# Optimization experiments

Measured on AMD Instinct MI355X. Metric: run time of the kernel, lower is better.

The kernel has to match this reference:

```python
import jax, jax.numpy as jnp
import numpy as np

B, L, D = 128, 196, 1024  # batch, att_size, rnn_size


def setup_inputs() -> dict:
    key = jax.random.key(0)
    ks = jax.random.split(key, 11)
    s = 1.0 / np.sqrt(D)
    return {
        "x": jax.random.normal(ks[0], (B, D), jnp.float32),
        "att": jax.random.normal(ks[1], (B, L, D), jnp.float32),
        "h": jax.random.normal(ks[2], (B, D), jnp.float32),
        "W_a2a": jax.random.uniform(ks[3], (D, D), jnp.float32, -s, s),
        "b_a2a": jax.random.uniform(ks[4], (D,), jnp.float32, -s, s),
        "W_h2a": jax.random.uniform(ks[5], (D, D), jnp.float32, -s, s),
        "b_h2a": jax.random.uniform(ks[6], (D,), jnp.float32, -s, s),
        "W_i2a": jax.random.uniform(ks[7], (D, D), jnp.float32, -s, s),
        "b_i2a": jax.random.uniform(ks[8], (D,), jnp.float32, -s, s),
        "W_d2d": jax.random.uniform(ks[9], (D,), jnp.float32, -s, s),
        "b_d2d": jax.random.uniform(ks[10], (), jnp.float32, -s, s),
    }


def reference(x, att, h, W_a2a, b_a2a, W_h2a, b_h2a, W_i2a, b_i2a, W_d2d, b_d2d):
    # att_v_1: [B, L, D]
    att_v = jnp.einsum('bld,ed->ble', att, W_a2a) + b_a2a
    att_h = (h @ W_h2a.T + b_h2a)[:, None, :]   # [B, 1, D]
    att_x = (x @ W_i2a.T + b_i2a)[:, None, :]   # [B, 1, D]
    dot = jnp.tanh(att_v + att_h + att_x)       # [B, L, D]
    scores = jnp.einsum('bld,d->bl', dot, W_d2d) + b_d2d  # [B, L]
    weight = jax.nn.softmax(scores, axis=-1)    # [B, L]
    att_res = jnp.einsum('bld,bl->bd', att, weight)  # [B, D]
    return att_res
```

## Files before the change

### kernel.cpp

```cpp
#include <hip/hip_runtime.h>
#include <hip/hip_bf16.h>

#define B_ 128
#define L_ 196
#define D_ 1024

typedef __attribute__((ext_vector_type(8))) short short8v;
typedef __attribute__((ext_vector_type(4))) float f32x4;
typedef unsigned short ushort_t;

#define OFF_ATTBF   0UL
#define OFF_WBF     51380224UL
#define OFF_A2      53477376UL
#define OFF_W2      54001664UL
#define OFF_SPART   53477376UL
#define OFF_CPART   58195968UL

__device__ inline unsigned short f2bf(float f) {
  unsigned int u = __float_as_uint(f);
  unsigned int r = (u + 0x7fffu + ((u >> 16) & 1u)) >> 16;
  return (unsigned short)r;
}

__global__ void convert_kernel(const float* __restrict__ att, const float* __restrict__ Wa,
                               const float* __restrict__ x,   const float* __restrict__ h,
                               const float* __restrict__ Wi,  const float* __restrict__ Wh,
                               ushort_t* __restrict__ att_bf, ushort_t* __restrict__ W_bf,
                               ushort_t* __restrict__ A2,     ushort_t* __restrict__ W2) {
  const int n0 = (B_*L_*D_)/4;
  const int n1 = (D_*D_)/4;
  const int n2 = (B_*D_)/4;
  const int total = n0 + n1 + 2*n2 + 2*n1;
  for (int idx = blockIdx.x*blockDim.x + threadIdx.x; idx < total;
       idx += gridDim.x*blockDim.x) {
    const float4* src; ushort_t* dst;
    int i = idx;
    if (i < n0)               { src = (const float4*)att + i; dst = att_bf + (size_t)i*4; }
    else if ((i -= n0) < n1)  { src = (const float4*)Wa  + i; dst = W_bf  + (size_t)i*4; }
    else if ((i -= n1) < n2)  { int b = i>>8, k4 = i&255; src = (const float4*)x  + i; dst = A2 + b*2048 + k4*4; }
    else if ((i -= n2) < n2)  { int b = i>>8, k4 = i&255; src = (const float4*)h  + i; dst = A2 + b*2048 + 1024 + k4*4; }
    else if ((i -= n2) < n1)  { int e = i>>8, k4 = i&255; src = (const float4*)Wi + i; dst = W2 + e*2048 + k4*4; }
    else { i -= n1;             int e = i>>8, k4 = i&255; src = (const float4*)Wh + i; dst = W2 + e*2048 + 1024 + k4*4; }
    float4 v = *src;
    ushort4 o; o.x = f2bf(v.x); o.y = f2bf(v.y); o.z = f2bf(v.z); o.w = f2bf(v.w);
    *(ushort4*)dst = o;
  }
}

__device__ inline void stage_tile(const ushort_t* __restrict__ g, int row0, int Kld, int k0,
                                  ushort_t* ldst, int t) {
  #pragma unroll
  for (int it = 0; it < 4; ++it) {
    int linear = it*4096 + t*16;
    int r = linear >> 7;
    int c = (t & 7) ^ (r & 7);
    const ushort_t* src = g + (size_t)(row0 + r)*Kld + k0 + c*8;
    ushort_t* dst = ldst + ((it*4096 + ((t & 192) << 4)) >> 1);
    __builtin_amdgcn_global_load_lds((const __attribute__((address_space(1))) void*)src,
                                     (__attribute__((address_space(3))) void*)dst,
                                     16, 0, 0);
  }
}

__device__ inline short8v ldfrag(const ushort_t* tile, int row, int c) {
  int phys = c ^ (row & 7);
  return *(const short8v*)(tile + row*64 + phys*8);
}

__global__ __launch_bounds__(256) void gemm_c_kernel(
    const ushort_t* __restrict__ Amat, const ushort_t* __restrict__ Bmat,
    float* __restrict__ cpart) {
  __shared__ ushort_t lds[32768];
  int bid = blockIdx.x;
  int e0 = (bid & 7)*128;
  int kc = bid >> 3;
  int kbeg = kc*512;
  const int Kld = 2048;
  int t = threadIdx.x, lane = t & 63, w = t >> 6;
  int wm = w >> 1, we = w & 1;
  int lrow = lane & 15;
  int lk = lane >> 4;

  f32x4 acc[4][4];
  #pragma unroll
  for (int i = 0; i < 4; ++i)
    #pragma unroll
    for (int j = 0; j < 4; ++j) acc[i][j] = (f32x4){0.f, 0.f, 0.f, 0.f};

  stage_tile(Amat, 0,  Kld, kbeg, lds, t);
  stage_tile(Bmat, e0, Kld, kbeg, lds + 8192, t);
  __syncthreads();

  const int nk = 8;
  for (int kt = 0; kt < nk; ++kt) {
    int cur = kt & 1;
    if (kt + 1 < nk) {
      stage_tile(Amat, 0,  Kld, kbeg + ((kt+1) << 6), lds + (cur^1)*16384, t);
      stage_tile(Bmat, e0, Kld, kbeg + ((kt+1) << 6), lds + (cur^1)*16384 + 8192, t);
    }
    const ushort_t* At = lds + cur*16384;
    const ushort_t* Bt = At + 8192;
    #pragma unroll
    for (int hh = 0; hh < 2; ++hh) {
      short8v af[4], bfv[4];
      #pragma unroll
      for (int i = 0; i < 4; ++i) af[i]  = ldfrag(At, wm*64 + i*16 + lrow, hh*4 + lk);
      #pragma unroll
      for (int j = 0; j < 4; ++j) bfv[j] = ldfrag(Bt, we*64 + j*16 + lrow, hh*4 + lk);
      #pragma unroll
      for (int i = 0; i < 4; ++i)
        #pragma unroll
        for (int j = 0; j < 4; ++j)
          acc[i][j] = __builtin_amdgcn_mfma_f32_16x16x32_bf16(af[i], bfv[j], acc[i][j], 0, 0, 0);
    }
    __syncthreads();
  }

  float* outc = cpart + (size_t)kc*131072;
  #pragma unroll
  for (int i = 0; i < 4; ++i) {
    int m = wm*64 + i*16 + lk*4;
    #pragma unroll
    for (int j = 0; j < 4; ++j) {
      int e = e0 + we*64 + j*16 + lrow;
      #pragma unroll
      for (int r = 0; r < 4; ++r)
        outc[(m + r)*1024 + e] = acc[i][j][r];
    }
  }
}

__device__ inline short8v ldfrag2(const ushort_t* tile, int row, int c) {
  int phys = c ^ (row & 7);
  return *(const short8v*)(tile + row*64 + phys*8);
}

#define STAGE(lanebase, half, kt, ldsT) { \
    const ushort_t* s0_ = (lanebase) + (half)*131072 + (kt)*64; \
    ushort_t* d0_ = (ldsT) + (half)*8192 + w*512; \
    __builtin_amdgcn_global_load_lds((const __attribute__((address_space(1))) void*)s0_, \
                                     (__attribute__((address_space(3))) void*)d0_, 16, 0, 0); \
    __builtin_amdgcn_global_load_lds((const __attribute__((address_space(1))) void*)(s0_ + 65536), \
                                     (__attribute__((address_space(3))) void*)(d0_ + 4096), 16, 0, 0); }

#define BARR()  __builtin_amdgcn_s_barrier()
#define VM6()   asm volatile("s_waitcnt vmcnt(6)" ::: "memory")

#define RD_A_LO(base) { _Pragma("unroll") for (int i_=0;i_<4;++i_) { int rr = wm*64 + i_*16 + lrow; \
    a[i_][0]=ldfrag2(base, rr, lk); a[i_][1]=ldfrag2(base, rr, 4+lk);} }
#define RD_A_HI(base) { _Pragma("unroll") for (int i_=0;i_<4;++i_) { int rr = 128 + wm*64 + i_*16 + lrow; \
    a[i_][0]=ldfrag2(base, rr, lk); a[i_][1]=ldfrag2(base, rr, 4+lk);} }
#define RD_B_LO(base) { _Pragma("unroll") for (int j_=0;j_<2;++j_) { int rr = wn*64 + j_*16 + lrow; \
    b[j_][0]=ldfrag2(base, rr, lk); b[j_][1]=ldfrag2(base, rr, 4+lk);} }
#define RD_B_HI(base) { _Pragma("unroll") for (int j_=0;j_<2;++j_) { int rr = wn*64 + (2+j_)*16 + lrow; \
    b[2+j_][0]=ldfrag2(base, rr, lk); b[2+j_][1]=ldfrag2(base, rr, 4+lk);} }

#define MFMAQ(I0, J0) { _Pragma("unroll") for (int k_=0;k_<2;++k_) { \
    _Pragma("unroll") for (int i_=0;i_<4;++i_) { _Pragma("unroll") for (int j_=0;j_<2;++j_) { \
      acc[(I0)+i_][(J0)+j_] = __builtin_amdgcn_mfma_f32_16x16x32_bf16(a[i_][k_], b[(J0)+j_][k_], acc[(I0)+i_][(J0)+j_], 0,0,0); } } } }

#define PH(I0, J0) BARR(); \
    __builtin_amdgcn_s_setprio(1); MFMAQ(I0, J0); __builtin_amdgcn_s_setprio(0);

__global__ __launch_bounds__(512, 2) void gemm_score_kernel(
    const ushort_t* __restrict__ Amat, const ushort_t* __restrict__ Bmat,
    const float* __restrict__ cpart,
    const float* __restrict__ ba, const float* __restrict__ bh, const float* __restrict__ bi,
    const float* __restrict__ wd,
    float* __restrict__ spart) {
  __shared__ ushort_t lds[65536];
  __shared__ float c_lds[768];
  const int nk = 16, NI = 8;
  int bid = blockIdx.x;
  int swz = (bid & 7)*49 + (bid >> 3);
  int m_blk = swz >> 2, e_blk = swz & 3;
  int m0 = m_blk*256, e0 = e_blk*256;
  int t = (int)threadIdx.x, lane = t & 63, w = t >> 6;
  int wm = w >> 2, wn = w & 3;
  int lrow = lane & 15, lk = lane >> 4;

  int bb0 = m0 / 196;
  for (int idx = t; idx < 768; idx += 512) {
    int bb = bb0 + (idx >> 8);
    int e  = e0 + (idx & 255);
    float v = ba[e] + bh[e] + bi[e];
    if (bb < 128) {
      v += cpart[bb*1024 + e] + cpart[131072 + bb*1024 + e]
         + cpart[262144 + bb*1024 + e] + cpart[393216 + bb*1024 + e];
    }
    c_lds[idx] = v;
  }

  int r0 = t >> 3;
  int c0 = (t & 7) ^ (r0 & 7);
  const ushort_t* aBase = Amat + (size_t)(m0 + r0)*1024 + c0*8;
  const ushort_t* bBase = Bmat + (size_t)(e0 + r0)*1024 + c0*8;

  ushort_t* A0_ = lds;
  ushort_t* B0_ = lds + 16384;
  ushort_t* A1_ = lds + 32768;
  ushort_t* B1_ = lds + 49152;

  f32x4 acc[8][4];
  #pragma unroll
  for (int i = 0; i < 8; ++i)
    #pragma unroll
    for (int j = 0; j < 4; ++j) acc[i][j] = (f32x4){0.f, 0.f, 0.f, 0.f};
  short8v a[4][2], b[4][2];

  STAGE(aBase, 0, 0, A0_);
  STAGE(aBase, 1, 0, A0_);
  STAGE(bBase, 0, 0, B0_);
  STAGE(bBase, 1, 0, B0_);
  STAGE(aBase, 0, 1, A1_);
  STAGE(bBase, 0, 1, B1_);
  STAGE(bBase, 1, 1, B1_);
  VM6(); BARR();

  for (int itr = 0; itr < NI; ++itr) {
    int kt0 = 2*itr;
    int kc2 = (kt0+2 < nk) ? kt0+2 : nk-1;
    int kc3 = (kt0+3 < nk) ? kt0+3 : nk-1;
    RD_A_LO(A0_); RD_B_LO(B0_);
    STAGE(aBase, 1, kt0+1, A1_);
    PH(0,0);
    RD_B_HI(B0_);
    PH(0,2);
    RD_A_HI(A0_);
    STAGE(aBase, 0, kc2, A0_);
    STAGE(bBase, 0, kc2, B0_);
    PH(4,0);
    STAGE(bBase, 1, kc2, B0_);
    VM6();
    PH(4,2);
    RD_A_LO(A1_); RD_B_LO(B1_);
    STAGE(aBase, 1, kc2, A0_);
    PH(0,0);
    RD_B_HI(B1_);
    PH(0,2);
    RD_A_HI(A1_);
    STAGE(aBase, 0, kc3, A1_);
    STAGE(bBase, 0, kc3, B1_);
    PH(4,0);
    STAGE(bBase, 1, kc3, B1_);
    VM6();
    PH(4,2);
  }

  int p = e_blk*4 + wn;
  #pragma unroll
  for (int i = 0; i < 8; ++i) {
    int mbase = m0 + (i>>2)*128 + wm*64 + (i&3)*16 + lk*4;
    f32x4 ps;
    #pragma unroll
    for (int r = 0; r < 4; ++r) {
      int m = mbase + r;
      int bb = (int)((unsigned)m / 196u);
      float partial = 0.f;
      #pragma unroll
      for (int j = 0; j < 4; ++j) {
        int ee = wn*64 + j*16 + lrow;
        float v = acc[i][j][r] + c_lds[(bb - bb0)*256 + ee];
        float ex = __expf(2.f*v);
        partial += (1.f - 2.f/(ex + 1.f)) * wd[e0 + ee];
      }
      partial += __shfl_xor(partial, 1);
      partial += __shfl_xor(partial, 2);
      partial += __shfl_xor(partial, 4);
      partial += __shfl_xor(partial, 8);
      ps[r] = partial;
    }
    if (lrow == 0) *(f32x4*)(spart + (size_t)p*25088 + mbase) = ps;
  }
}

__global__ __launch_bounds__(256) void finalize_kernel(const ushort_t* __restrict__ att_bf,
                                                       const float* __restrict__ spart,
                                                       float* __restrict__ out) {
  int b  = blockIdx.x >> 1;
  int dh = blockIdx.x & 1;
  int t  = threadIdx.x;
  __shared__ float wls[L_];
  __shared__ float red[8];

  float s = -1e30f;
  if (t < L_) {
    int m = b*L_ + t;
    float sum = 0.f;
    #pragma unroll
    for (int p = 0; p < 16; ++p) sum += spart[p*25088 + m];
    s = sum;
  }
  float mx = s;
  #pragma unroll
  for (int off = 1; off < 64; off <<= 1) mx = fmaxf(mx, __shfl_xor(mx, off));
  if ((t & 63) == 0) red[t >> 6] = mx;
  __syncthreads();
  mx = fmaxf(fmaxf(red[0], red[1]), fmaxf(red[2], red[3]));
  float pr = (t < L_) ? __expf(s - mx) : 0.f;
  float ssum = pr;
  #pragma unroll
  for (int off = 1; off < 64; off <<= 1) ssum += __shfl_xor(ssum, off);
  if ((t & 63) == 0) red[4 + (t >> 6)] = ssum;
  __syncthreads();
  float tot = red[4] + red[5] + red[6] + red[7];
  if (t < L_) wls[t] = pr / tot;
  __syncthreads();

  int d = dh*512 + t*2;
  const ushort_t* abase = att_bf + (size_t)b*L_*D_ + d;
  float a0 = 0.f, a1 = 0.f;
  #pragma unroll 4
  for (int l = 0; l < L_; ++l) {
    float wv = wls[l];
    unsigned int v = *(const unsigned int*)(abase + (size_t)l*D_);
    float lo = __uint_as_float(v << 16);
    float hi = __uint_as_float(v & 0xffff0000u);
    a0 += wv*lo; a1 += wv*hi;
  }
  float2 o; o.x = a0; o.y = a1;
  *(float2*)(out + (size_t)b*D_ + d) = o;
}

extern "C" void kernel_launch(void* const* d_in, const int* in_sizes, int n_in,
                              void* d_out, int out_size, void* d_ws, size_t ws_size,
                              hipStream_t stream) {
  (void)in_sizes; (void)n_in; (void)out_size; (void)ws_size;
  const float* x   = (const float*)d_in[0];
  const float* att = (const float*)d_in[1];
  const float* h   = (const float*)d_in[2];
  const float* Wa  = (const float*)d_in[3];
  const float* ba  = (const float*)d_in[4];
  const float* Wh  = (const float*)d_in[5];
  const float* bh  = (const float*)d_in[6];
  const float* Wi  = (const float*)d_in[7];
  const float* bi  = (const float*)d_in[8];
  const float* wd  = (const float*)d_in[9];

  char* ws = (char*)d_ws;
  ushort_t* att_bf = (ushort_t*)(ws + OFF_ATTBF);
  ushort_t* W_bf   = (ushort_t*)(ws + OFF_WBF);
  ushort_t* A2     = (ushort_t*)(ws + OFF_A2);
  ushort_t* W2     = (ushort_t*)(ws + OFF_W2);
  float*    cpart  = (float*)(ws + OFF_CPART);
  float*    spart  = (float*)(ws + OFF_SPART);
  float*    out    = (float*)d_out;

  hipLaunchKernelGGL(convert_kernel, dim3(2048), dim3(256), 0, stream,
                     att, Wa, x, h, Wi, Wh, att_bf, W_bf, A2, W2);
  hipLaunchKernelGGL(gemm_c_kernel, dim3(32), dim3(256), 0, stream,
                     A2, W2, cpart);
  hipLaunchKernelGGL(gemm_score_kernel, dim3(392), dim3(512), 0, stream,
                     att_bf, W_bf, cpart, ba, bh, bi, wd, spart);
  hipLaunchKernelGGL(finalize_kernel, dim3(256), dim3(256), 0, stream,
                     att_bf, spart, out);
}
```

Baseline: 125.7 us.

## Replace fine-grained interleaved GEMM pipeline with simple double-buffered k-tile loop

```diff
diff --git a/kernel.cpp b/kernel.cpp
--- a/kernel.cpp
+++ b/kernel.cpp
@@ -144,23 +144,29 @@
                                      (__attribute__((address_space(3))) void*)(d0_ + 4096), 16, 0, 0); }
 
 #define BARR()  __builtin_amdgcn_s_barrier()
-#define VM6()   asm volatile("s_waitcnt vmcnt(6)" ::: "memory")
-
-#define RD_A_LO(base) { _Pragma("unroll") for (int i_=0;i_<4;++i_) { int rr = wm*64 + i_*16 + lrow; \
-    a[i_][0]=ldfrag2(base, rr, lk); a[i_][1]=ldfrag2(base, rr, 4+lk);} }
-#define RD_A_HI(base) { _Pragma("unroll") for (int i_=0;i_<4;++i_) { int rr = 128 + wm*64 + i_*16 + lrow; \
-    a[i_][0]=ldfrag2(base, rr, lk); a[i_][1]=ldfrag2(base, rr, 4+lk);} }
-#define RD_B_LO(base) { _Pragma("unroll") for (int j_=0;j_<2;++j_) { int rr = wn*64 + j_*16 + lrow; \
-    b[j_][0]=ldfrag2(base, rr, lk); b[j_][1]=ldfrag2(base, rr, 4+lk);} }
-#define RD_B_HI(base) { _Pragma("unroll") for (int j_=0;j_<2;++j_) { int rr = wn*64 + (2+j_)*16 + lrow; \
-    b[2+j_][0]=ldfrag2(base, rr, lk); b[2+j_][1]=ldfrag2(base, rr, 4+lk);} }
-
-#define MFMAQ(I0, J0) { _Pragma("unroll") for (int k_=0;k_<2;++k_) { \
+#define VM8()   asm volatile("s_waitcnt vmcnt(8)" ::: "memory")
+
+#define RD_ALO_K(base, kk) { _Pragma("unroll") for (int i_=0;i_<4;++i_) \
+    aLo[i_][kk] = ldfrag2(base, wm*64 + i_*16 + lrow, (kk)*4 + lk); }
+#define RD_AHI_K(base, kk) { _Pragma("unroll") for (int i_=0;i_<4;++i_) \
+    aHi[i_][kk] = ldfrag2(base, 128 + wm*64 + i_*16 + lrow, (kk)*4 + lk); }
+#define RD_B01_K(base, kk) { _Pragma("unroll") for (int j_=0;j_<2;++j_) \
+    b01[j_][kk] = ldfrag2(base, wn*64 + j_*16 + lrow, (kk)*4 + lk); }
+#define RD_B23_K(base, kk) { _Pragma("unroll") for (int j_=0;j_<2;++j_) \
+    b23[j_][kk] = ldfrag2(base, wn*64 + (2+j_)*16 + lrow, (kk)*4 + lk); }
+
+#define MQ(I0, J0, A_, B_) { _Pragma("unroll") for (int k_=0;k_<2;++k_) { \
     _Pragma("unroll") for (int i_=0;i_<4;++i_) { _Pragma("unroll") for (int j_=0;j_<2;++j_) { \
-      acc[(I0)+i_][(J0)+j_] = __builtin_amdgcn_mfma_f32_16x16x32_bf16(a[i_][k_], b[(J0)+j_][k_], acc[(I0)+i_][(J0)+j_], 0,0,0); } } } }
-
-#define PH(I0, J0) BARR(); \
-    __builtin_amdgcn_s_setprio(1); MFMAQ(I0, J0); __builtin_amdgcn_s_setprio(0);
+      acc[(I0)+i_][(J0)+j_] = __builtin_amdgcn_mfma_f32_16x16x32_bf16(A_[i_][k_], B_[j_][k_], acc[(I0)+i_][(J0)+j_], 0,0,0); } } } }
+
+#define KTILE_BODY(Abuf, Bbuf) \
+    RD_ALO_K(Abuf, 0); RD_B01_K(Bbuf, 0); RD_B23_K(Bbuf, 0); \
+    RD_ALO_K(Abuf, 1); RD_B01_K(Bbuf, 1); RD_B23_K(Bbuf, 1); \
+    MQ(0, 0, aLo, b01); \
+    RD_AHI_K(Abuf, 0); RD_AHI_K(Abuf, 1); \
+    MQ(0, 2, aLo, b23); \
+    MQ(4, 0, aHi, b01); \
+    MQ(4, 2, aHi, b23);
 
 __global__ __launch_bounds__(512, 2) void gemm_score_kernel(
     const ushort_t* __restrict__ Amat, const ushort_t* __restrict__ Bmat,
@@ -170,7 +176,7 @@
     float* __restrict__ spart) {
   __shared__ ushort_t lds[65536];
   __shared__ float c_lds[768];
-  const int nk = 16, NI = 8;
+  const int nk = 16;
   int bid = blockIdx.x;
   int swz = (bid & 7)*49 + (bid >> 3);
   int m_blk = swz >> 2, e_blk = swz & 3;
@@ -206,45 +212,29 @@
   for (int i = 0; i < 8; ++i)
     #pragma unroll
     for (int j = 0; j < 4; ++j) acc[i][j] = (f32x4){0.f, 0.f, 0.f, 0.f};
-  short8v a[4][2], b[4][2];
-
-  STAGE(aBase, 0, 0, A0_);
-  STAGE(aBase, 1, 0, A0_);
-  STAGE(bBase, 0, 0, B0_);
-  STAGE(bBase, 1, 0, B0_);
-  STAGE(aBase, 0, 1, A1_);
-  STAGE(bBase, 0, 1, B1_);
-  STAGE(bBase, 1, 1, B1_);
-  VM6(); BARR();
-
-  for (int itr = 0; itr < NI; ++itr) {
-    int kt0 = 2*itr;
-    int kc2 = (kt0+2 < nk) ? kt0+2 : nk-1;
-    int kc3 = (kt0+3 < nk) ? kt0+3 : nk-1;
-    RD_A_LO(A0_); RD_B_LO(B0_);
-    STAGE(aBase, 1, kt0+1, A1_);
-    PH(0,0);
-    RD_B_HI(B0_);
-    PH(0,2);
-    RD_A_HI(A0_);
-    STAGE(aBase, 0, kc2, A0_);
-    STAGE(bBase, 0, kc2, B0_);
-    PH(4,0);
-    STAGE(bBase, 1, kc2, B0_);
-    VM6();
-    PH(4,2);
-    RD_A_LO(A1_); RD_B_LO(B1_);
-    STAGE(aBase, 1, kc2, A0_);
-    PH(0,0);
-    RD_B_HI(B1_);
-    PH(0,2);
-    RD_A_HI(A1_);
-    STAGE(aBase, 0, kc3, A1_);
-    STAGE(bBase, 0, kc3, B1_);
-    PH(4,0);
-    STAGE(bBase, 1, kc3, B1_);
-    VM6();
-    PH(4,2);
+  short8v aLo[4][2], aHi[4][2], b01[2][2], b23[2][2];
+
+  STAGE(aBase, 0, 0, A0_); STAGE(aBase, 1, 0, A0_);
+  STAGE(bBase, 0, 0, B0_); STAGE(bBase, 1, 0, B0_);
+  STAGE(aBase, 0, 1, A1_); STAGE(aBase, 1, 1, A1_);
+  STAGE(bBase, 0, 1, B1_); STAGE(bBase, 1, 1, B1_);
+
+  for (int it2 = 0; it2 < 8; ++it2) {
+    int kt = 2*it2;
+    VM8();
+    BARR();
+    KTILE_BODY(A0_, B0_);
+    BARR();
+    { int ks = (kt+2 < nk) ? kt+2 : nk-1;
+      STAGE(aBase, 0, ks, A0_); STAGE(aBase, 1, ks, A0_);
+      STAGE(bBase, 0, ks, B0_); STAGE(bBase, 1, ks, B0_); }
+    VM8();
+    BARR();
+    KTILE_BODY(A1_, B1_);
+    BARR();
+    { int ks = (kt+3 < nk) ? kt+3 : nk-1;
+      STAGE(aBase, 0, ks, A1_); STAGE(aBase, 1, ks, A1_);
+      STAGE(bBase, 0, ks, B1_); STAGE(bBase, 1, ks, B1_); }
   }
 
   int p = e_blk*4 + wn;
```

Measured after the change: 126.2 us. About the same (+0.4%).

## Fuse x/h/Wi/Wh bf16 conversion into small GEMM and split K wider

Applied to the files above, without the earlier changes.

```diff
diff --git a/kernel.cpp b/kernel.cpp
--- a/kernel.cpp
+++ b/kernel.cpp
@@ -11,10 +11,8 @@
 
 #define OFF_ATTBF   0UL
 #define OFF_WBF     51380224UL
-#define OFF_A2      53477376UL
-#define OFF_W2      54001664UL
 #define OFF_SPART   53477376UL
-#define OFF_CPART   58195968UL
+#define OFF_CPART   55083008UL
 
 __device__ inline unsigned short f2bf(float f) {
   unsigned int u = __float_as_uint(f);
@@ -23,42 +21,22 @@
 }
 
 __global__ void convert_kernel(const float* __restrict__ att, const float* __restrict__ Wa,
-                               const float* __restrict__ x,   const float* __restrict__ h,
-                               const float* __restrict__ Wi,  const float* __restrict__ Wh,
-                               ushort_t* __restrict__ att_bf, ushort_t* __restrict__ W_bf,
-                               ushort_t* __restrict__ A2,     ushort_t* __restrict__ W2) {
-  const int n0 = (B_*L_*D_)/4;
-  const int n1 = (D_*D_)/4;
-  const int n2 = (B_*D_)/4;
-  const int total = n0 + n1 + 2*n2 + 2*n1;
+                               ushort_t* __restrict__ att_bf, ushort_t* __restrict__ W_bf) {
+  const int n0 = (B_*L_*D_)/8;
+  const int n1 = (D_*D_)/8;
+  const int total = n0 + n1;
   for (int idx = blockIdx.x*blockDim.x + threadIdx.x; idx < total;
        idx += gridDim.x*blockDim.x) {
-    const float4* src; ushort_t* dst;
-    int i = idx;
-    if (i < n0)               { src = (const float4*)att + i; dst = att_bf + (size_t)i*4; }
-    else if ((i -= n0) < n1)  { src = (const float4*)Wa  + i; dst = W_bf  + (size_t)i*4; }
-    else if ((i -= n1) < n2)  { int b = i>>8, k4 = i&255; src = (const float4*)x  + i; dst = A2 + b*2048 + k4*4; }
-    else if ((i -= n2) < n2)  { int b = i>>8, k4 = i&255; src = (const float4*)h  + i; dst = A2 + b*2048 + 1024 + k4*4; }
-    else if ((i -= n2) < n1)  { int e = i>>8, k4 = i&255; src = (const float4*)Wi + i; dst = W2 + e*2048 + k4*4; }
-    else { i -= n1;             int e = i>>8, k4 = i&255; src = (const float4*)Wh + i; dst = W2 + e*2048 + 1024 + k4*4; }
-    float4 v = *src;
-    ushort4 o; o.x = f2bf(v.x); o.y = f2bf(v.y); o.z = f2bf(v.z); o.w = f2bf(v.w);
-    *(ushort4*)dst = o;
-  }
-}
-
-__device__ inline void stage_tile(const ushort_t* __restrict__ g, int row0, int Kld, int k0,
-                                  ushort_t* ldst, int t) {
-  #pragma unroll
-  for (int it = 0; it < 4; ++it) {
-    int linear = it*4096 + t*16;
-    int r = linear >> 7;
-    int c = (t & 7) ^ (r & 7);
-    const ushort_t* src = g + (size_t)(row0 + r)*Kld + k0 + c*8;
-    ushort_t* dst = ldst + ((it*4096 + ((t & 192) << 4)) >> 1);
-    __builtin_amdgcn_global_load_lds((const __attribute__((address_space(1))) void*)src,
-                                     (__attribute__((address_space(3))) void*)dst,
-                                     16, 0, 0);
+    const float4* s; ushort_t* d;
+    if (idx < n0) { s = (const float4*)att + (size_t)idx*2; d = att_bf + (size_t)idx*8; }
+    else { int i = idx - n0; s = (const float4*)Wa + (size_t)i*2; d = W_bf + (size_t)i*8; }
+    float4 f0 = s[0], f1 = s[1];
+    short8v o;
+    o[0] = (short)f2bf(f0.x); o[1] = (short)f2bf(f0.y);
+    o[2] = (short)f2bf(f0.z); o[3] = (short)f2bf(f0.w);
+    o[4] = (short)f2bf(f1.x); o[5] = (short)f2bf(f1.y);
+    o[6] = (short)f2bf(f1.z); o[7] = (short)f2bf(f1.w);
+    *(short8v*)d = o;
   }
 }
 
@@ -68,18 +46,19 @@
 }
 
 __global__ __launch_bounds__(256) void gemm_c_kernel(
-    const ushort_t* __restrict__ Amat, const ushort_t* __restrict__ Bmat,
+    const float* __restrict__ x, const float* __restrict__ h,
+    const float* __restrict__ Wi, const float* __restrict__ Wh,
     float* __restrict__ cpart) {
-  __shared__ ushort_t lds[32768];
+  __shared__ ushort_t lds[16384];
   int bid = blockIdx.x;
   int e0 = (bid & 7)*128;
   int kc = bid >> 3;
-  int kbeg = kc*512;
-  const int Kld = 2048;
+  const float* Asrc = (kc < 4) ? x : h;
+  const float* Bsrc = (kc < 4) ? Wi : Wh;
+  int kb = (kc & 3)*256;
   int t = threadIdx.x, lane = t & 63, w = t >> 6;
   int wm = w >> 1, we = w & 1;
-  int lrow = lane & 15;
-  int lk = lane >> 4;
+  int lrow = lane & 15, lk = lane >> 4;
 
   f32x4 acc[4][4];
   #pragma unroll
@@ -87,26 +66,34 @@
     #pragma unroll
     for (int j = 0; j < 4; ++j) acc[i][j] = (f32x4){0.f, 0.f, 0.f, 0.f};
 
-  stage_tile(Amat, 0,  Kld, kbeg, lds, t);
-  stage_tile(Bmat, e0, Kld, kbeg, lds + 8192, t);
-  __syncthreads();
-
-  const int nk = 8;
-  for (int kt = 0; kt < nk; ++kt) {
-    int cur = kt & 1;
-    if (kt + 1 < nk) {
-      stage_tile(Amat, 0,  Kld, kbeg + ((kt+1) << 6), lds + (cur^1)*16384, t);
-      stage_tile(Bmat, e0, Kld, kbeg + ((kt+1) << 6), lds + (cur^1)*16384 + 8192, t);
-    }
-    const ushort_t* At = lds + cur*16384;
-    const ushort_t* Bt = At + 8192;
+  for (int kt = 0; kt < 4; ++kt) {
+    int k0 = kb + (kt << 6);
+    #pragma unroll
+    for (int q = 0; q < 4; ++q) {
+      int li = t*4 + q;
+      int r = li >> 3, c = li & 7;
+      int phys = (c ^ (r & 7))*8;
+      const float* sA = Asrc + r*1024 + k0 + c*8;
+      float4 a0 = *(const float4*)sA, a1 = *(const float4*)(sA + 4);
+      short8v oa;
+      oa[0]=(short)f2bf(a0.x); oa[1]=(short)f2bf(a0.y); oa[2]=(short)f2bf(a0.z); oa[3]=(short)f2bf(a0.w);
+      oa[4]=(short)f2bf(a1.x); oa[5]=(short)f2bf(a1.y); oa[6]=(short)f2bf(a1.z); oa[7]=(short)f2bf(a1.w);
+      *(short8v*)(lds + r*64 + phys) = oa;
+      const float* sB = Bsrc + (size_t)(e0 + r)*1024 + k0 + c*8;
+      float4 b0 = *(const float4*)sB, b1 = *(const float4*)(sB + 4);
+      short8v ob;
+      ob[0]=(short)f2bf(b0.x); ob[1]=(short)f2bf(b0.y); ob[2]=(short)f2bf(b0.z); ob[3]=(short)f2bf(b0.w);
+      ob[4]=(short)f2bf(b1.x); ob[5]=(short)f2bf(b1.y); ob[6]=(short)f2bf(b1.z); ob[7]=(short)f2bf(b1.w);
+      *(short8v*)(lds + 8192 + r*64 + phys) = ob;
+    }
+    __syncthreads();
     #pragma unroll
     for (int hh = 0; hh < 2; ++hh) {
       short8v af[4], bfv[4];
       #pragma unroll
-      for (int i = 0; i < 4; ++i) af[i]  = ldfrag(At, wm*64 + i*16 + lrow, hh*4 + lk);
-      #pragma unroll
-      for (int j = 0; j < 4; ++j) bfv[j] = ldfrag(Bt, we*64 + j*16 + lrow, hh*4 + lk);
+      for (int i = 0; i < 4; ++i) af[i]  = ldfrag(lds, wm*64 + i*16 + lrow, hh*4 + lk);
+      #pragma unroll
+      for (int j = 0; j < 4; ++j) bfv[j] = ldfrag(lds + 8192, we*64 + j*16 + lrow, hh*4 + lk);
       #pragma unroll
       for (int i = 0; i < 4; ++i)
         #pragma unroll
@@ -128,11 +115,6 @@
         outc[(m + r)*1024 + e] = acc[i][j][r];
     }
   }
-}
-
-__device__ inline short8v ldfrag2(const ushort_t* tile, int row, int c) {
-  int phys = c ^ (row & 7);
-  return *(const short8v*)(tile + row*64 + phys*8);
 }
 
 #define STAGE(lanebase, half, kt, ldsT) { \
@@ -146,14 +128,18 @@
 #define BARR()  __builtin_amdgcn_s_barrier()
 #define VM6()   asm volatile("s_waitcnt vmcnt(6)" ::: "memory")
 
-#define RD_A_LO(base) { _Pragma("unroll") for (int i_=0;i_<4;++i_) { int rr = wm*64 + i_*16 + lrow; \
-    a[i_][0]=ldfrag2(base, rr, lk); a[i_][1]=ldfrag2(base, rr, 4+lk);} }
-#define RD_A_HI(base) { _Pragma("unroll") for (int i_=0;i_<4;++i_) { int rr = 128 + wm*64 + i_*16 + lrow; \
-    a[i_][0]=ldfrag2(base, rr, lk); a[i_][1]=ldfrag2(base, rr, 4+lk);} }
-#define RD_B_LO(base) { _Pragma("unroll") for (int j_=0;j_<2;++j_) { int rr = wn*64 + j_*16 + lrow; \
-    b[j_][0]=ldfrag2(base, rr, lk); b[j_][1]=ldfrag2(base, rr, 4+lk);} }
-#define RD_B_HI(base) { _Pragma("unroll") for (int j_=0;j_<2;++j_) { int rr = wn*64 + (2+j_)*16 + lrow; \
-    b[2+j_][0]=ldfrag2(base, rr, lk); b[2+j_][1]=ldfrag2(base, rr, 4+lk);} }
+#define RD_A_LO(P0, P1) { _Pragma("unroll") for (int i_=0;i_<4;++i_) { \
+    a[i_][0] = *(const short8v*)((P0) + i_*1024); \
+    a[i_][1] = *(const short8v*)((P1) + i_*1024); } }
+#define RD_A_HI(P0, P1) { _Pragma("unroll") for (int i_=0;i_<4;++i_) { \
+    a[i_][0] = *(const short8v*)((P0) + 8192 + i_*1024); \
+    a[i_][1] = *(const short8v*)((P1) + 8192 + i_*1024); } }
+#define RD_B_LO(P0, P1) { _Pragma("unroll") for (int j_=0;j_<2;++j_) { \
+    b[j_][0] = *(const short8v*)((P0) + j_*1024); \
+    b[j_][1] = *(const short8v*)((P1) + j_*1024); } }
+#define RD_B_HI(P0, P1) { _Pragma("unroll") for (int j_=0;j_<2;++j_) { \
+    b[2+j_][0] = *(const short8v*)((P0) + (2+j_)*1024); \
+    b[2+j_][1] = *(const short8v*)((P1) + (2+j_)*1024); } }
 
 #define MFMAQ(I0, J0) { _Pragma("unroll") for (int k_=0;k_<2;++k_) { \
     _Pragma("unroll") for (int i_=0;i_<4;++i_) { _Pragma("unroll") for (int j_=0;j_<2;++j_) { \
@@ -170,7 +156,7 @@
     float* __restrict__ spart) {
   __shared__ ushort_t lds[65536];
   __shared__ float c_lds[768];
-  const int nk = 16, NI = 8;
+  const int nk = 16;
   int bid = blockIdx.x;
   int swz = (bid & 7)*49 + (bid >> 3);
   int m_blk = swz >> 2, e_blk = swz & 3;
@@ -185,8 +171,8 @@
     int e  = e0 + (idx & 255);
     float v = ba[e] + bh[e] + bi[e];
     if (bb < 128) {
-      v += cpart[bb*1024 + e] + cpart[131072 + bb*1024 + e]
-         + cpart[262144 + bb*1024 + e] + cpart[393216 + bb*1024 + e];
+      #pragma unroll
+      for (int p = 0; p < 8; ++p) v += cpart[p*131072 + bb*1024 + e];
     }
     c_lds[idx] = v;
   }
@@ -200,6 +186,18 @@
   ushort_t* B0_ = lds + 16384;
   ushort_t* A1_ = lds + 32768;
   ushort_t* B1_ = lds + 49152;
+
+  int lrow7 = lrow & 7;
+  int offk0 = ((lk)     ^ lrow7)*8;
+  int offk1 = ((4 + lk) ^ lrow7)*8;
+  const ushort_t* pA00 = lds + (wm*64 + lrow)*64 + offk0;
+  const ushort_t* pA01 = lds + (wm*64 + lrow)*64 + offk1;
+  const ushort_t* pA10 = pA00 + 32768;
+  const ushort_t* pA11 = pA01 + 32768;
+  const ushort_t* pB00 = lds + 16384 + (wn*64 + lrow)*64 + offk0;
+  const ushort_t* pB01 = lds + 16384 + (wn*64 + lrow)*64 + offk1;
+  const ushort_t* pB10 = pB00 + 32768;
+  const ushort_t* pB11 = pB01 + 32768;
 
   f32x4 acc[8][4];
   #pragma unroll
@@ -217,28 +215,28 @@
   STAGE(bBase, 1, 1, B1_);
   VM6(); BARR();
 
-  for (int itr = 0; itr < NI; ++itr) {
+  for (int itr = 0; itr < 8; ++itr) {
     int kt0 = 2*itr;
     int kc2 = (kt0+2 < nk) ? kt0+2 : nk-1;
     int kc3 = (kt0+3 < nk) ? kt0+3 : nk-1;
-    RD_A_LO(A0_); RD_B_LO(B0_);
+    RD_A_LO(pA00, pA01); RD_B_LO(pB00, pB01);
     STAGE(aBase, 1, kt0+1, A1_);
     PH(0,0);
-    RD_B_HI(B0_);
+    RD_B_HI(pB00, pB01);
     PH(0,2);
-    RD_A_HI(A0_);
+    RD_A_HI(pA00, pA01);
     STAGE(aBase, 0, kc2, A0_);
     STAGE(bBase, 0, kc2, B0_);
     PH(4,0);
     STAGE(bBase, 1, kc2, B0_);
     VM6();
     PH(4,2);
-    RD_A_LO(A1_); RD_B_LO(B1_);
+    RD_A_LO(pA10, pA11); RD_B_LO(pB10, pB11);
     STAGE(aBase, 1, kc2, A0_);
     PH(0,0);
-    RD_B_HI(B1_);
+    RD_B_HI(pB10, pB11);
     PH(0,2);
-    RD_A_HI(A1_);
+    RD_A_HI(pA10, pA11);
     STAGE(aBase, 0, kc3, A1_);
     STAGE(bBase, 0, kc3, B1_);
     PH(4,0);
@@ -340,16 +338,14 @@
   char* ws = (char*)d_ws;
   ushort_t* att_bf = (ushort_t*)(ws + OFF_ATTBF);
   ushort_t* W_bf   = (ushort_t*)(ws + OFF_WBF);
-  ushort_t* A2     = (ushort_t*)(ws + OFF_A2);
-  ushort_t* W2     = (ushort_t*)(ws + OFF_W2);
+  float*    spart  = (float*)(ws + OFF_SPART);
   float*    cpart  = (float*)(ws + OFF_CPART);
-  float*    spart  = (float*)(ws + OFF_SPART);
   float*    out    = (float*)d_out;
 
   hipLaunchKernelGGL(convert_kernel, dim3(2048), dim3(256), 0, stream,
-                     att, Wa, x, h, Wi, Wh, att_bf, W_bf, A2, W2);
-  hipLaunchKernelGGL(gemm_c_kernel, dim3(32), dim3(256), 0, stream,
-                     A2, W2, cpart);
+                     att, Wa, att_bf, W_bf);
+  hipLaunchKernelGGL(gemm_c_kernel, dim3(64), dim3(256), 0, stream,
+                     x, h, Wi, Wh, cpart);
   hipLaunchKernelGGL(gemm_score_kernel, dim3(392), dim3(512), 0, stream,
                      att_bf, W_bf, cpart, ba, bh, bi, wd, spart);
   hipLaunchKernelGGL(finalize_kernel, dim3(256), dim3(256), 0, stream,
```

New measurement: 132.6 us. 5.5% more time.
